# Optimization experiments

Hardware: AMD Instinct MI355X
Metric: run time of the kernel (lower is better)

## Reference

```python
import jax, jax.numpy as jnp
import numpy as np

N_NODES = 100000
N_EDGES = 50000   # number of hyperedges
NNZ = 500000      # incidence entries
IN_C = 128
OUT_C = 128


def setup_inputs() -> dict:
    key = jax.random.key(0)
    k1, k2, k3, k4 = jax.random.split(key, 4)
    x = jax.random.normal(k1, (N_NODES, IN_C), dtype=jnp.float32)
    node_idx = jax.random.randint(k2, (NNZ,), 0, N_NODES, dtype=jnp.int32)
    edge_idx = jax.random.randint(k3, (NNZ,), 0, N_EDGES, dtype=jnp.int32)
    hyperedge_index = jnp.stack([node_idx, edge_idx], axis=0)  # [2, NNZ]
    W = jax.random.normal(k4, (IN_C, OUT_C), dtype=jnp.float32) / np.sqrt(IN_C).astype(np.float32)
    b = jnp.zeros((OUT_C,), dtype=jnp.float32)
    return {"x": x, "hyperedge_index": hyperedge_index, "W": W, "b": b}


def reference(x, hyperedge_index, W, b):
    # PyG HypergraphConv (use_attention=False, heads=1, unit hyperedge weights):
    #   out = D^{-1} H B^{-1} H^T (X W) + b
    node_idx = hyperedge_index[0]  # [NNZ] node index of each incidence
    edge_idx = hyperedge_index[1]  # [NNZ] hyperedge index of each incidence

    xw = x @ W  # [N_NODES, OUT_C]

    ones = jnp.ones(node_idx.shape[0], dtype=xw.dtype)
    deg_n = jax.ops.segment_sum(ones, node_idx, num_segments=N_NODES)  # D
    d_inv = jnp.where(deg_n > 0, 1.0 / deg_n, 0.0)
    deg_e = jax.ops.segment_sum(ones, edge_idx, num_segments=N_EDGES)  # B
    b_inv = jnp.where(deg_e > 0, 1.0 / deg_e, 0.0)

    # node -> hyperedge: m_e = B^{-1}_e * sum_{v in e} xw_v
    edge_feat = jax.ops.segment_sum(xw[node_idx], edge_idx, num_segments=N_EDGES)
    edge_feat = edge_feat * b_inv[:, None]  # [N_EDGES, OUT_C]

    # hyperedge -> node: out_v = D^{-1}_v * sum_{e \ni v} m_e
    out = jax.ops.segment_sum(edge_feat[edge_idx], node_idx, num_segments=N_NODES)
    out = out * d_inv[:, None]  # [N_NODES, OUT_C]

    return out + b
```

## Files before the change

### kernel.cpp

```cpp
#include <hip/hip_runtime.h>

typedef unsigned short u16;
typedef unsigned int u32;

#define N_NODES 100000
#define N_EDGES 50000
#define C 128
#define G_GEMM 1563
#define NCNT (N_EDGES + N_NODES)
#define NBUCKC 1172
#define BCHUNK 2048

static __device__ __forceinline__ float bf2f(u16 h) {
    u32 u = ((u32)h) << 16;
    float f;
    __builtin_memcpy(&f, &u, 4);
    return f;
}

static __device__ __forceinline__ u16 f2bf(float f) {
    u32 u;
    __builtin_memcpy(&u, &f, 4);
    return (u16)((u + 0x7fffu + ((u >> 16) & 1u)) >> 16);
}

typedef short s16x8 __attribute__((ext_vector_type(8)));
typedef float f32x4 __attribute__((ext_vector_type(4)));

__global__ void transpose_w(const float* __restrict__ W, u16* __restrict__ Wt) {
    int idx = blockIdx.x * 256 + threadIdx.x;
    int k = idx >> 7, oc = idx & 127;
    Wt[oc * 128 + k] = f2bf(W[k * 128 + oc]);
}

__global__ __launch_bounds__(256) void gemm_k(
    const float* __restrict__ x, const u16* __restrict__ Wt,
    u16* __restrict__ xw) {
    __shared__ float xs[64 * C];
    int tid = threadIdx.x;
    int blk = blockIdx.x;
    int lane = tid & 63;
    int wave = tid >> 6;

    size_t gbase = (size_t)blk * 64 * C;
#pragma unroll
    for (int rnd = 0; rnd < 8; ++rnd) {
        int fl = rnd * 1024 + wave * 256 + lane * 4;
        int grow = blk * 64 + (fl >> 7);
        const float* src = (grow < N_NODES) ? (x + gbase + fl) : x;
        __builtin_amdgcn_global_load_lds(
            (const __attribute__((address_space(1))) void*)src,
            (__attribute__((address_space(3))) void*)(xs + rnd * 1024 + wave * 256),
            16, 0, 0);
    }
    __syncthreads();

    int tile = blk * 4 + wave;
    if (tile >= 6250) return;
    int m = lane & 15;
    int quad = lane >> 4;
    int row0 = tile * 16;

    const float* xr = xs + (wave * 16 + m) * C + quad * 8;
    f32x4 acc[8];
#pragma unroll
    for (int nt = 0; nt < 8; ++nt) acc[nt] = (f32x4){0.f, 0.f, 0.f, 0.f};

    union { uint4 u; s16x8 v; } a[4];
#pragma unroll
    for (int kk = 0; kk < 4; ++kk) {
        float4 v0 = *(const float4*)(xr + kk * 32);
        float4 v1 = *(const float4*)(xr + kk * 32 + 4);
        a[kk].u.x = (u32)f2bf(v0.x) | ((u32)f2bf(v0.y) << 16);
        a[kk].u.y = (u32)f2bf(v0.z) | ((u32)f2bf(v0.w) << 16);
        a[kk].u.z = (u32)f2bf(v1.x) | ((u32)f2bf(v1.y) << 16);
        a[kk].u.w = (u32)f2bf(v1.z) | ((u32)f2bf(v1.w) << 16);
    }

#pragma unroll
    for (int kk = 0; kk < 4; ++kk) {
        int kb = kk * 32 + quad * 8;
#pragma unroll
        for (int nt = 0; nt < 8; ++nt) {
            union { uint4 u; s16x8 v; } b;
            b.u = *(const uint4*)(Wt + (size_t)(nt * 16 + m) * C + kb);
            acc[nt] = __builtin_amdgcn_mfma_f32_16x16x32_bf16(a[kk].v, b.v, acc[nt], 0, 0, 0);
        }
    }

#pragma unroll
    for (int nt = 0; nt < 8; ++nt) {
#pragma unroll
        for (int r = 0; r < 4; ++r) {
            int row = row0 + quad * 4 + r;
            xw[(size_t)row * C + nt * 16 + m] = f2bf(acc[nt][r]);
        }
    }
}

__global__ __launch_bounds__(256) void bucket_hist_k(
    const int* __restrict__ ni, const int* __restrict__ ei,
    u32* __restrict__ cntM, int nnz, int nb1) {
    __shared__ u32 h[NBUCKC];
    for (int b = threadIdx.x; b < NBUCKC; b += 256) h[b] = 0;
    __syncthreads();
    int i0 = blockIdx.x * BCHUNK;
    int iend = min(i0 + BCHUNK, nnz);
    for (int i = i0 + threadIdx.x; i < iend; i += 256) {
        int e = ei[i], n = ni[i];
        atomicAdd(&h[e >> 7], 1u);
        atomicAdd(&h[(N_EDGES + n) >> 7], 1u);
    }
    __syncthreads();
    for (int b = threadIdx.x; b < NBUCKC; b += 256)
        cntM[(size_t)b * nb1 + blockIdx.x] = h[b];
}

__global__ __launch_bounds__(256) void scan_a2(const u32* __restrict__ cnt,
                                               u32* __restrict__ off,
                                               u32* __restrict__ bsum, int N) {
    __shared__ u32 wsum[4];
    int tid = threadIdx.x;
    int base = blockIdx.x * 1024 + tid * 4;
    u32 v0 = 0, v1 = 0, v2 = 0, v3 = 0;
    if (base + 3 < N) {
        uint4 v = *(const uint4*)(cnt + base);
        v0 = v.x; v1 = v.y; v2 = v.z; v3 = v.w;
    } else {
        if (base + 0 < N) v0 = cnt[base + 0];
        if (base + 1 < N) v1 = cnt[base + 1];
        if (base + 2 < N) v2 = cnt[base + 2];
        if (base + 3 < N) v3 = cnt[base + 3];
    }
    u32 s = v0 + v1 + v2 + v3;
    int lane = tid & 63, wv = tid >> 6;
    u32 x = s;
    for (int d = 1; d < 64; d <<= 1) {
        u32 y = __shfl_up(x, (unsigned)d);
        if (lane >= d) x += y;
    }
    if (lane == 63) wsum[wv] = x;
    __syncthreads();
    u32 wo = 0;
    for (int w = 0; w < 4; ++w) wo += (w < wv) ? wsum[w] : 0u;
    u32 ex = wo + x - s;
    if (base + 0 < N) off[base + 0] = ex;
    if (base + 1 < N) off[base + 1] = ex + v0;
    if (base + 2 < N) off[base + 2] = ex + v0 + v1;
    if (base + 3 < N) off[base + 3] = ex + v0 + v1 + v2;
    if (tid == 255) bsum[blockIdx.x] = wo + x;
}

__global__ __launch_bounds__(256) void scan_b2(u32* __restrict__ bsum, int nb) {
    __shared__ u32 wsum[4];
    int t = threadIdx.x;
    u32 v0 = (2 * t < nb) ? bsum[2 * t] : 0u;
    u32 v1 = (2 * t + 1 < nb) ? bsum[2 * t + 1] : 0u;
    u32 s = v0 + v1;
    int lane = t & 63, wv = t >> 6;
    u32 x = s;
    for (int d = 1; d < 64; d <<= 1) {
        u32 y = __shfl_up(x, (unsigned)d);
        if (lane >= d) x += y;
    }
    if (lane == 63) wsum[wv] = x;
    __syncthreads();
    u32 wo = 0;
    for (int w = 0; w < 4; ++w) wo += (w < wv) ? wsum[w] : 0u;
    u32 ex = wo + x - s;
    if (2 * t < nb) bsum[2 * t] = ex;
    if (2 * t + 1 < nb) bsum[2 * t + 1] = ex + v0;
}

__global__ __launch_bounds__(256) void bucket_place_k(
    const int* __restrict__ ni, const int* __restrict__ ei,
    const u32* __restrict__ offM, const u32* __restrict__ bsum,
    u32* __restrict__ stage, int nnz, int nb1) {
    __shared__ u32 cur[NBUCKC];
    for (int b = threadIdx.x; b < NBUCKC; b += 256) {
        size_t idx = (size_t)b * nb1 + blockIdx.x;
        cur[b] = offM[idx] + bsum[idx >> 10];
    }
    __syncthreads();
    int i0 = blockIdx.x * BCHUNK;
    int iend = min(i0 + BCHUNK, nnz);
    for (int i = i0 + threadIdx.x; i < iend; i += 256) {
        int e = ei[i], n = ni[i];
        u32 p1 = atomicAdd(&cur[e >> 7], 1u);
        stage[p1] = ((u32)(e & 127) << 17) | (u32)n;
        int k2 = N_EDGES + n;
        u32 p2 = atomicAdd(&cur[k2 >> 7], 1u);
        stage[p2] = ((u32)(k2 & 127) << 17) | (u32)e;
    }
}

__global__ __launch_bounds__(256) void bucket_csr_k(
    const u32* __restrict__ offM, const u32* __restrict__ bsum,
    const u32* __restrict__ stage, u32* __restrict__ csr,
    uint2* __restrict__ rowinfo, int nnz, int nb1) {
    __shared__ u32 h[128];
    __shared__ u32 ks[128];
    int b = blockIdx.x;
    size_t i0 = (size_t)b * nb1;
    u32 gstart = offM[i0] + bsum[i0 >> 10];
    u32 gend;
    if (b + 1 < NBUCKC) {
        size_t i1 = (size_t)(b + 1) * nb1;
        gend = offM[i1] + bsum[i1 >> 10];
    } else {
        gend = (u32)(2 * nnz);
    }
    int size = (int)(gend - gstart);
    if (threadIdx.x < 128) h[threadIdx.x] = 0;
    __syncthreads();
    for (int i = threadIdx.x; i < size; i += 256)
        atomicAdd(&h[stage[gstart + i] >> 17], 1u);
    __syncthreads();
    if (threadIdx.x < 64) {
        int l = threadIdx.x;
        u32 s0 = h[2 * l], s1 = h[2 * l + 1];
        u32 ps = s0 + s1;
        u32 x = ps;
        for (int d = 1; d < 64; d <<= 1) {
            u32 y = __shfl_up(x, (unsigned)d);
            if (l >= d) x += y;
        }
        u32 ex = x - ps;
        ks[2 * l] = ex;
        ks[2 * l + 1] = ex + s0;
        int gk = b * 128 + 2 * l;
        if (gk < NCNT) rowinfo[gk] = make_uint2(gstart + ex, s0);
        if (gk + 1 < NCNT) rowinfo[gk + 1] = make_uint2(gstart + ex + s0, s1);
    }
    __syncthreads();
    for (int i = threadIdx.x; i < size; i += 256) {
        u32 en = stage[gstart + i];
        u32 kl = en >> 17;
        u32 p = atomicAdd(&ks[kl], 1u);
        csr[gstart + p] = en & 0x1FFFFu;
    }
}

#define GATHER8(SRC)                                                          \
    for (u32 base = 0; base < deg; base += 64) {                              \
        int m = (int)min(64u, deg - base);                                    \
        int myidx = (lane < m) ? (int)csr[start + base + lane] : 0;           \
        for (int t = 0; t < m; t += 8) {                                      \
            int i1 = min(t + 1, m - 1), i2 = min(t + 2, m - 1);               \
            int i3 = min(t + 3, m - 1), i4 = min(t + 4, m - 1);               \
            int i5 = min(t + 5, m - 1), i6 = min(t + 6, m - 1);               \
            int i7 = min(t + 7, m - 1);                                       \
            int r0 = __shfl(myidx, t),  r1 = __shfl(myidx, i1);               \
            int r2 = __shfl(myidx, i2), r3 = __shfl(myidx, i3);               \
            int r4 = __shfl(myidx, i4), r5 = __shfl(myidx, i5);               \
            int r6 = __shfl(myidx, i6), r7 = __shfl(myidx, i7);               \
            u32 u0 = ((const u32*)(SRC + (size_t)r0 * C))[lane];              \
            u32 u1 = ((const u32*)(SRC + (size_t)r1 * C))[lane];              \
            u32 u2 = ((const u32*)(SRC + (size_t)r2 * C))[lane];              \
            u32 u3 = ((const u32*)(SRC + (size_t)r3 * C))[lane];              \
            u32 u4 = ((const u32*)(SRC + (size_t)r4 * C))[lane];              \
            u32 u5 = ((const u32*)(SRC + (size_t)r5 * C))[lane];              \
            u32 u6 = ((const u32*)(SRC + (size_t)r6 * C))[lane];              \
            u32 u7 = ((const u32*)(SRC + (size_t)r7 * C))[lane];              \
            float k1 = (t + 1 < m) ? 1.f : 0.f, k2 = (t + 2 < m) ? 1.f : 0.f; \
            float k3 = (t + 3 < m) ? 1.f : 0.f, k4 = (t + 4 < m) ? 1.f : 0.f; \
            float k5 = (t + 5 < m) ? 1.f : 0.f, k6 = (t + 6 < m) ? 1.f : 0.f; \
            float k7 = (t + 7 < m) ? 1.f : 0.f;                               \
            ax += bf2f((u16)(u0 & 0xffffu)) + k1 * bf2f((u16)(u1 & 0xffffu))  \
                + k2 * bf2f((u16)(u2 & 0xffffu)) + k3 * bf2f((u16)(u3 & 0xffffu)) \
                + k4 * bf2f((u16)(u4 & 0xffffu)) + k5 * bf2f((u16)(u5 & 0xffffu)) \
                + k6 * bf2f((u16)(u6 & 0xffffu)) + k7 * bf2f((u16)(u7 & 0xffffu)); \
            ay += bf2f((u16)(u0 >> 16)) + k1 * bf2f((u16)(u1 >> 16))          \
                + k2 * bf2f((u16)(u2 >> 16)) + k3 * bf2f((u16)(u3 >> 16))     \
                + k4 * bf2f((u16)(u4 >> 16)) + k5 * bf2f((u16)(u5 >> 16))     \
                + k6 * bf2f((u16)(u6 >> 16)) + k7 * bf2f((u16)(u7 >> 16));    \
        }                                                                     \
    }

__global__ __launch_bounds__(256) void edge_gather_k(const u16* __restrict__ xw,
                                                     const uint2* __restrict__ rowinfo,
                                                     const u32* __restrict__ csrC,
                                                     u16* __restrict__ ef) {
    int e = blockIdx.x * 4 + (threadIdx.x >> 6);
    if (e >= N_EDGES) return;
    int lane = threadIdx.x & 63;
    uint2 ri = rowinfo[e];
    u32 deg = ri.y;
    u32 start = ri.x;
    const u32* csr = csrC;
    float ax = 0.f, ay = 0.f;
    GATHER8(xw)
    float sc = deg ? 1.f / (float)deg : 0.f;
    ((u32*)(ef + (size_t)e * C))[lane] =
        (u32)f2bf(ax * sc) | ((u32)f2bf(ay * sc) << 16);
}

__global__ __launch_bounds__(256) void node_gather_k(const u16* __restrict__ ef,
                                                     const uint2* __restrict__ rowinfo,
                                                     const u32* __restrict__ csrC,
                                                     const float* __restrict__ bias,
                                                     float* __restrict__ out) {
    int v = blockIdx.x * 4 + (threadIdx.x >> 6);
    if (v >= N_NODES) return;
    int lane = threadIdx.x & 63;
    uint2 ri = rowinfo[N_EDGES + v];
    u32 deg = ri.y;
    u32 start = ri.x;
    const u32* csr = csrC;
    float ax = 0.f, ay = 0.f;
    GATHER8(ef)
    float b0 = bias[2 * lane], b1 = bias[2 * lane + 1];
    float sc = deg ? 1.f / (float)deg : 0.f;
    float2 r;
    r.x = ax * sc + b0;
    r.y = ay * sc + b1;
    ((float2*)(out + (size_t)v * C))[lane] = r;
}

extern "C" void kernel_launch(void* const* d_in, const int* in_sizes, int n_in,
                              void* d_out, int out_size, void* d_ws, size_t ws_size,
                              hipStream_t stream) {
    const float* x = (const float*)d_in[0];
    const int* node_idx = (const int*)d_in[1];
    const int nnz = in_sizes[1] / 2;
    const int* edge_idx = node_idx + nnz;
    const float* W = (const float*)d_in[2];
    const float* bias = (const float*)d_in[3];
    float* out = (float*)d_out;

    int nb1 = (nnz + BCHUNK - 1) / BCHUNK;
    int scanN = NBUCKC * nb1;
    int scanBlocks = (scanN + 1023) / 1024;

    u16* Wt = (u16*)d_ws;
    u16* ef = Wt + 16384;
    u32* cntM = (u32*)(ef + (size_t)N_EDGES * C);
    u32* offM = cntM + scanN;
    u32* bsum2 = offM + scanN;
    uint2* rowinfo = (uint2*)(bsum2 + 512);
    u32* csrC = (u32*)(rowinfo + NCNT);

    u16* xw = (u16*)d_out;
    u32* stage = (u32*)((char*)d_out + (size_t)N_NODES * C * 2);

    transpose_w<<<64, 256, 0, stream>>>(W, Wt);
    gemm_k<<<G_GEMM, 256, 0, stream>>>(x, Wt, xw);
    bucket_hist_k<<<nb1, 256, 0, stream>>>(node_idx, edge_idx, cntM, nnz, nb1);
    scan_a2<<<scanBlocks, 256, 0, stream>>>(cntM, offM, bsum2, scanN);
    scan_b2<<<1, 256, 0, stream>>>(bsum2, scanBlocks);
    bucket_place_k<<<nb1, 256, 0, stream>>>(node_idx, edge_idx, offM, bsum2,
                                            stage, nnz, nb1);
    bucket_csr_k<<<NBUCKC, 256, 0, stream>>>(offM, bsum2, stage, csrC, rowinfo,
                                             nnz, nb1);
    edge_gather_k<<<(N_EDGES + 3) / 4, 256, 0, stream>>>(xw, rowinfo, csrC, ef);
    node_gather_k<<<(N_NODES + 3) / 4, 256, 0, stream>>>(ef, rowinfo, csrC, bias, out);
}
```

Baseline: 215.7 us.

## Stage GEMM output through LDS and split gathers into half-wave 8-byte loads

The GEMM epilogue now writes the bf16 results to shared memory and then stores them to global memory as coalesced 16-byte vectors, replacing scattered 2-byte stores. The edge and node gather kernels give each half-wave a separate incidence, and each lane loads 8 bytes (4 channels) instead of 4. The two halves are combined with a cross-half shuffle at the end, and the outputs are written as wider vectors. This targets memory-transaction efficiency and doubles the number of independent rows in flight per wave. The cost is extra barriers and shuffles, and half the lanes sit idle during the final store.

Result: no change. 212.9 us (-1.3%).

```diff
diff --git a/kernel.cpp b/kernel.cpp
--- a/kernel.cpp
+++ b/kernel.cpp
@@ -36,7 +36,7 @@
 __global__ __launch_bounds__(256) void gemm_k(
     const float* __restrict__ x, const u16* __restrict__ Wt,
     u16* __restrict__ xw) {
-    __shared__ float xs[64 * C];
+    __shared__ __align__(16) float xs[64 * C];
     int tid = threadIdx.x;
     int blk = blockIdx.x;
     int lane = tid & 63;
@@ -56,45 +56,54 @@
     __syncthreads();
 
     int tile = blk * 4 + wave;
-    if (tile >= 6250) return;
     int m = lane & 15;
     int quad = lane >> 4;
-    int row0 = tile * 16;
-
-    const float* xr = xs + (wave * 16 + m) * C + quad * 8;
-    f32x4 acc[8];
-#pragma unroll
-    for (int nt = 0; nt < 8; ++nt) acc[nt] = (f32x4){0.f, 0.f, 0.f, 0.f};
+    bool live = (tile < 6250);
 
     union { uint4 u; s16x8 v; } a[4];
-#pragma unroll
-    for (int kk = 0; kk < 4; ++kk) {
-        float4 v0 = *(const float4*)(xr + kk * 32);
-        float4 v1 = *(const float4*)(xr + kk * 32 + 4);
-        a[kk].u.x = (u32)f2bf(v0.x) | ((u32)f2bf(v0.y) << 16);
-        a[kk].u.y = (u32)f2bf(v0.z) | ((u32)f2bf(v0.w) << 16);
-        a[kk].u.z = (u32)f2bf(v1.x) | ((u32)f2bf(v1.y) << 16);
-        a[kk].u.w = (u32)f2bf(v1.z) | ((u32)f2bf(v1.w) << 16);
-    }
-
-#pragma unroll
-    for (int kk = 0; kk < 4; ++kk) {
-        int kb = kk * 32 + quad * 8;
-#pragma unroll
-        for (int nt = 0; nt < 8; ++nt) {
-            union { uint4 u; s16x8 v; } b;
-            b.u = *(const uint4*)(Wt + (size_t)(nt * 16 + m) * C + kb);
-            acc[nt] = __builtin_amdgcn_mfma_f32_16x16x32_bf16(a[kk].v, b.v, acc[nt], 0, 0, 0);
+    if (live) {
+        const float* xr = xs + (wave * 16 + m) * C + quad * 8;
+#pragma unroll
+        for (int kk = 0; kk < 4; ++kk) {
+            float4 v0 = *(const float4*)(xr + kk * 32);
+            float4 v1 = *(const float4*)(xr + kk * 32 + 4);
+            a[kk].u.x = (u32)f2bf(v0.x) | ((u32)f2bf(v0.y) << 16);
+            a[kk].u.y = (u32)f2bf(v0.z) | ((u32)f2bf(v0.w) << 16);
+            a[kk].u.z = (u32)f2bf(v1.x) | ((u32)f2bf(v1.y) << 16);
+            a[kk].u.w = (u32)f2bf(v1.z) | ((u32)f2bf(v1.w) << 16);
         }
     }
-
-#pragma unroll
-    for (int nt = 0; nt < 8; ++nt) {
-#pragma unroll
-        for (int r = 0; r < 4; ++r) {
-            int row = row0 + quad * 4 + r;
-            xw[(size_t)row * C + nt * 16 + m] = f2bf(acc[nt][r]);
+    __syncthreads();
+
+    u16* ct = (u16*)xs;
+    if (live) {
+        f32x4 acc[8];
+#pragma unroll
+        for (int nt = 0; nt < 8; ++nt) acc[nt] = (f32x4){0.f, 0.f, 0.f, 0.f};
+#pragma unroll
+        for (int kk = 0; kk < 4; ++kk) {
+            int kb = kk * 32 + quad * 8;
+#pragma unroll
+            for (int nt = 0; nt < 8; ++nt) {
+                union { uint4 u; s16x8 v; } b;
+                b.u = *(const uint4*)(Wt + (size_t)(nt * 16 + m) * C + kb);
+                acc[nt] = __builtin_amdgcn_mfma_f32_16x16x32_bf16(a[kk].v, b.v, acc[nt], 0, 0, 0);
+            }
         }
+#pragma unroll
+        for (int nt = 0; nt < 8; ++nt)
+#pragma unroll
+            for (int r = 0; r < 4; ++r)
+                ct[(wave * 16 + quad * 4 + r) * C + nt * 16 + m] = f2bf(acc[nt][r]);
+    }
+    __syncthreads();
+
+#pragma unroll
+    for (int r = 0; r < 4; ++r) {
+        int f = r * 2048 + tid * 8;
+        int grow = blk * 64 + (f >> 7);
+        if (grow < N_NODES)
+            *(uint4*)(xw + (size_t)blk * 64 * C + f) = *(const uint4*)(ct + f);
     }
 }
 
@@ -241,41 +250,37 @@
     }
 }
 
-#define GATHER8(SRC)                                                          \
+#define GATHERP(SRC)                                                          \
     for (u32 base = 0; base < deg; base += 64) {                              \
         int m = (int)min(64u, deg - base);                                    \
         int myidx = (lane < m) ? (int)csr[start + base + lane] : 0;           \
         for (int t = 0; t < m; t += 8) {                                      \
-            int i1 = min(t + 1, m - 1), i2 = min(t + 2, m - 1);               \
-            int i3 = min(t + 3, m - 1), i4 = min(t + 4, m - 1);               \
-            int i5 = min(t + 5, m - 1), i6 = min(t + 6, m - 1);               \
-            int i7 = min(t + 7, m - 1);                                       \
-            int r0 = __shfl(myidx, t),  r1 = __shfl(myidx, i1);               \
-            int r2 = __shfl(myidx, i2), r3 = __shfl(myidx, i3);               \
-            int r4 = __shfl(myidx, i4), r5 = __shfl(myidx, i5);               \
-            int r6 = __shfl(myidx, i6), r7 = __shfl(myidx, i7);               \
-            u32 u0 = ((const u32*)(SRC + (size_t)r0 * C))[lane];              \
-            u32 u1 = ((const u32*)(SRC + (size_t)r1 * C))[lane];              \
-            u32 u2 = ((const u32*)(SRC + (size_t)r2 * C))[lane];              \
-            u32 u3 = ((const u32*)(SRC + (size_t)r3 * C))[lane];              \
-            u32 u4 = ((const u32*)(SRC + (size_t)r4 * C))[lane];              \
-            u32 u5 = ((const u32*)(SRC + (size_t)r5 * C))[lane];              \
-            u32 u6 = ((const u32*)(SRC + (size_t)r6 * C))[lane];              \
-            u32 u7 = ((const u32*)(SRC + (size_t)r7 * C))[lane];              \
-            float k1 = (t + 1 < m) ? 1.f : 0.f, k2 = (t + 2 < m) ? 1.f : 0.f; \
-            float k3 = (t + 3 < m) ? 1.f : 0.f, k4 = (t + 4 < m) ? 1.f : 0.f; \
-            float k5 = (t + 5 < m) ? 1.f : 0.f, k6 = (t + 6 < m) ? 1.f : 0.f; \
-            float k7 = (t + 7 < m) ? 1.f : 0.f;                               \
-            ax += bf2f((u16)(u0 & 0xffffu)) + k1 * bf2f((u16)(u1 & 0xffffu))  \
-                + k2 * bf2f((u16)(u2 & 0xffffu)) + k3 * bf2f((u16)(u3 & 0xffffu)) \
-                + k4 * bf2f((u16)(u4 & 0xffffu)) + k5 * bf2f((u16)(u5 & 0xffffu)) \
-                + k6 * bf2f((u16)(u6 & 0xffffu)) + k7 * bf2f((u16)(u7 & 0xffffu)); \
-            ay += bf2f((u16)(u0 >> 16)) + k1 * bf2f((u16)(u1 >> 16))          \
-                + k2 * bf2f((u16)(u2 >> 16)) + k3 * bf2f((u16)(u3 >> 16))     \
-                + k4 * bf2f((u16)(u4 >> 16)) + k5 * bf2f((u16)(u5 >> 16))     \
-                + k6 * bf2f((u16)(u6 >> 16)) + k7 * bf2f((u16)(u7 >> 16));    \
+            int e0 = min(t + 0 + half, m - 1), e1 = min(t + 2 + half, m - 1); \
+            int e2 = min(t + 4 + half, m - 1), e3 = min(t + 6 + half, m - 1); \
+            int r0 = __shfl(myidx, e0), r1 = __shfl(myidx, e1);               \
+            int r2 = __shfl(myidx, e2), r3 = __shfl(myidx, e3);               \
+            uint2 u0 = ((const uint2*)(SRC + (size_t)r0 * C))[ch];            \
+            uint2 u1 = ((const uint2*)(SRC + (size_t)r1 * C))[ch];            \
+            uint2 u2 = ((const uint2*)(SRC + (size_t)r2 * C))[ch];            \
+            uint2 u3 = ((const uint2*)(SRC + (size_t)r3 * C))[ch];            \
+            float m0 = (t + 0 + half < m) ? 1.f : 0.f;                        \
+            float m1 = (t + 2 + half < m) ? 1.f : 0.f;                        \
+            float m2 = (t + 4 + half < m) ? 1.f : 0.f;                        \
+            float m3 = (t + 6 + half < m) ? 1.f : 0.f;                        \
+            a0 += m0 * bf2f((u16)(u0.x & 0xffffu)) + m1 * bf2f((u16)(u1.x & 0xffffu)) \
+                + m2 * bf2f((u16)(u2.x & 0xffffu)) + m3 * bf2f((u16)(u3.x & 0xffffu)); \
+            a1 += m0 * bf2f((u16)(u0.x >> 16)) + m1 * bf2f((u16)(u1.x >> 16)) \
+                + m2 * bf2f((u16)(u2.x >> 16)) + m3 * bf2f((u16)(u3.x >> 16)); \
+            a2 += m0 * bf2f((u16)(u0.y & 0xffffu)) + m1 * bf2f((u16)(u1.y & 0xffffu)) \
+                + m2 * bf2f((u16)(u2.y & 0xffffu)) + m3 * bf2f((u16)(u3.y & 0xffffu)); \
+            a3 += m0 * bf2f((u16)(u0.y >> 16)) + m1 * bf2f((u16)(u1.y >> 16)) \
+                + m2 * bf2f((u16)(u2.y >> 16)) + m3 * bf2f((u16)(u3.y >> 16)); \
         }                                                                     \
-    }
+    }                                                                         \
+    a0 += __shfl_xor(a0, 32);                                                 \
+    a1 += __shfl_xor(a1, 32);                                                 \
+    a2 += __shfl_xor(a2, 32);                                                 \
+    a3 += __shfl_xor(a3, 32);
 
 __global__ __launch_bounds__(256) void edge_gather_k(const u16* __restrict__ xw,
                                                      const uint2* __restrict__ rowinfo,
@@ -284,15 +289,20 @@
     int e = blockIdx.x * 4 + (threadIdx.x >> 6);
     if (e >= N_EDGES) return;
     int lane = threadIdx.x & 63;
+    int half = lane >> 5, ch = lane & 31;
     uint2 ri = rowinfo[e];
     u32 deg = ri.y;
     u32 start = ri.x;
     const u32* csr = csrC;
-    float ax = 0.f, ay = 0.f;
-    GATHER8(xw)
+    float a0 = 0.f, a1 = 0.f, a2 = 0.f, a3 = 0.f;
+    GATHERP(xw)
     float sc = deg ? 1.f / (float)deg : 0.f;
-    ((u32*)(ef + (size_t)e * C))[lane] =
-        (u32)f2bf(ax * sc) | ((u32)f2bf(ay * sc) << 16);
+    if (lane < 32) {
+        uint2 w;
+        w.x = (u32)f2bf(a0 * sc) | ((u32)f2bf(a1 * sc) << 16);
+        w.y = (u32)f2bf(a2 * sc) | ((u32)f2bf(a3 * sc) << 16);
+        ((uint2*)(ef + (size_t)e * C))[ch] = w;
+    }
 }
 
 __global__ __launch_bounds__(256) void node_gather_k(const u16* __restrict__ ef,
@@ -303,18 +313,23 @@
     int v = blockIdx.x * 4 + (threadIdx.x >> 6);
     if (v >= N_NODES) return;
     int lane = threadIdx.x & 63;
+    int half = lane >> 5, ch = lane & 31;
     uint2 ri = rowinfo[N_EDGES + v];
     u32 deg = ri.y;
     u32 start = ri.x;
     const u32* csr = csrC;
-    float ax = 0.f, ay = 0.f;
-    GATHER8(ef)
-    float b0 = bias[2 * lane], b1 = bias[2 * lane + 1];
+    float a0 = 0.f, a1 = 0.f, a2 = 0.f, a3 = 0.f;
+    GATHERP(ef)
     float sc = deg ? 1.f / (float)deg : 0.f;
-    float2 r;
-    r.x = ax * sc + b0;
-    r.y = ay * sc + b1;
-    ((float2*)(out + (size_t)v * C))[lane] = r;
+    if (lane < 32) {
+        float4 bv = *(const float4*)(bias + ch * 4);
+        float4 w;
+        w.x = a0 * sc + bv.x;
+        w.y = a1 * sc + bv.y;
+        w.z = a2 * sc + bv.z;
+        w.w = a3 * sc + bv.w;
+        ((float4*)(out + (size_t)v * C))[ch] = w;
+    }
 }
 
 extern "C" void kernel_launch(void* const* d_in, const int* in_sizes, int n_in,
```
